# Kernel optimization log

Measured on AMD Instinct MI355X. Metric: run time of the kernel, lower is better.

## Reference

```python
import jax, jax.numpy as jnp
import numpy as np

P_PARTS = 6
NUM_CLASSES = 50000
BATCH = 128
PART_DIM = 256
LABEL_SMOOTH = 0.1
MARGIN = 0.3
TEMP = 3.0
KL_CLAMP = 5.0
LAMBDA_GRAPH = 0.1
LAMBDA_TRI = 1.0
LAMBDA_ADV = 0.1
START_EPOCH = 20


def setup_inputs() -> dict:
    key = jax.random.key(0)
    ks = jax.random.split(key, 8)
    id_logits = jax.random.normal(ks[0], (P_PARTS, BATCH, NUM_CLASSES), dtype=jnp.float32)
    id_features = jax.random.normal(ks[1], (P_PARTS, BATCH, PART_DIM), dtype=jnp.float32)
    gray_features = jax.random.normal(ks[2], (P_PARTS, BATCH, PART_DIM), dtype=jnp.float32)
    # soft labels are probability distributions (teacher softmax outputs)
    soft_labels = jax.nn.softmax(jax.random.normal(ks[3], (P_PARTS, BATCH, NUM_CLASSES), dtype=jnp.float32), axis=-1)
    entropy_weights = jax.random.uniform(ks[4], (P_PARTS, BATCH), dtype=jnp.float32)
    adv_logits = jax.random.normal(ks[5], (P_PARTS, BATCH, 2), dtype=jnp.float32)
    labels = jax.random.randint(ks[6], (BATCH,), 0, 16, dtype=jnp.int64 if jax.config.jax_enable_x64 else jnp.int32)
    modality_labels = jax.random.randint(ks[7], (BATCH,), 0, 2, dtype=jnp.int64 if jax.config.jax_enable_x64 else jnp.int32)
    return {
        'id_logits': id_logits,
        'id_features': id_features,
        'gray_features': gray_features,
        'soft_labels': soft_labels,
        'entropy_weights': entropy_weights,
        'adv_logits': adv_logits,
        'labels': labels,
        'modality_labels': modality_labels,
        'current_epoch': 25,
    }


def _ce(logits, labels, smoothing):
    # torch CrossEntropyLoss with label_smoothing, mean reduction. logits: [B,C]
    logp = jax.nn.log_softmax(logits, axis=-1)
    nll = -jnp.take_along_axis(logp, labels[:, None], axis=-1)[:, 0]
    smooth = -jnp.mean(logp, axis=-1)
    return jnp.mean((1.0 - smoothing) * nll + smoothing * smooth)


def _triplet(feat, target_feat, labels, same):
    # euclidean cdist [B,B]
    sq = (jnp.sum(feat * feat, axis=1)[:, None]
          + jnp.sum(target_feat * target_feat, axis=1)[None, :]
          - 2.0 * feat @ target_feat.T)
    dist = jnp.sqrt(jnp.clip(sq, 0.0) + 1e-12)
    eq = labels[:, None] == labels[None, :]
    is_neg = ~eq
    is_pos = eq & (~jnp.eye(feat.shape[0], dtype=bool)) if same else eq
    # vectorized hard mining (replaces per-row python loop)
    dist_ap = jnp.where(is_pos.any(axis=1),
                        jnp.max(jnp.where(is_pos, dist, -jnp.inf), axis=1), 0.0)
    dist_an = jnp.where(is_neg.any(axis=1),
                        jnp.min(jnp.where(is_neg, dist, jnp.inf), axis=1), 1e6)
    # MarginRankingLoss with y=1: mean(relu(dist_ap - dist_an + margin))
    return jnp.mean(jnp.maximum(dist_ap - dist_an + MARGIN, 0.0))


def reference(id_logits, id_features, gray_features, soft_labels, entropy_weights,
              adv_logits, labels, modality_labels, current_epoch):
    P = id_logits.shape[0]
    # --- multi-part ID loss ---
    L_id = jnp.mean(jax.vmap(lambda lg: _ce(lg, labels, LABEL_SMOOTH))(id_logits))
    # --- triplet on L2-normalized concatenated part features ---
    feat = jnp.concatenate(list(id_features), axis=1)  # [B, P*D]
    feat = feat / jnp.linalg.norm(feat, axis=1, keepdims=True)
    L_tri = _triplet(feat, feat, labels, same=True)
    feat_gray = jnp.concatenate(list(gray_features), axis=1)
    feat_gray = feat_gray / jnp.linalg.norm(feat_gray, axis=1, keepdims=True)
    L_trans = _triplet(feat, feat_gray, labels, same=False)
    L_tri = L_tri + 0.5 * L_trans
    # --- graph distillation (KL) ---
    if current_epoch >= START_EPOCH:
        logp = jax.nn.log_softmax(id_logits / TEMP, axis=-1)  # [P,B,C]
        kl = jnp.sum(soft_labels * (jnp.log(soft_labels) - logp), axis=-1)  # [P,B]
        kl = jnp.minimum(kl, KL_CLAMP)
        L_graph = jnp.sum(jnp.mean(kl * entropy_weights, axis=1)) * (TEMP ** 2) / P
    else:
        L_graph = jnp.float32(0.0)
    # --- adversarial CE ---
    logp_adv = jax.nn.log_softmax(adv_logits, axis=-1)  # [P,B,2]
    nll_adv = -jnp.take_along_axis(logp_adv, modality_labels[None, :, None], axis=-1)[..., 0]
    L_adv = jnp.mean(jnp.mean(nll_adv, axis=1))
    total = L_id + LAMBDA_TRI * L_tri + LAMBDA_GRAPH * L_graph + LAMBDA_ADV * L_adv
    return total
```

## Files before the change

kernel.cpp:

```cpp
#include <hip/hip_runtime.h>

#define NCLS   50000
#define NC4    12500
#define BATCH  128
#define PPARTS 6
#define NROWS  768
#define FD     1536
#define NCHUNK 5
#define C4     2500

__device__ __forceinline__ float wave_sum(float v) {
#pragma unroll
  for (int off = 32; off > 0; off >>= 1) v += __shfl_xor(v, off, 64);
  return v;
}

__global__ __launch_bounds__(128) void chunk_k(
    const float* __restrict__ X, const float* __restrict__ S,
    const int* __restrict__ labels, float* __restrict__ P) {
  const int gid = blockIdx.x;
  const int row = gid / NCHUNK;
  const int ch  = gid - row * NCHUNK;
  const int b   = row & (BATCH - 1);
  const int t   = threadIdx.x;
  const size_t base = (size_t)row * NCLS;
  const float4* x4 = (const float4*)(X + base) + ch * C4;
  const float4* s4 = (const float4*)(S + base) + ch * C4;
  const float i3 = 1.0f / 3.0f;

  float xl = 0.0f;
  if (ch == 0 && t == 0) xl = X[base + labels[b]];

  float m = -1e30f, e1 = 0.0f, e2 = 0.0f;
  float sx = 0.0f, ss = 0.0f, ssl = 0.0f, ssx = 0.0f;

  float4 xa = make_float4(0.f, 0.f, 0.f, 0.f), sa = xa, xb = xa, sb = xa;
  if (t < C4) { xa = x4[t]; sa = s4[t]; }
  if (t + 128 < C4) { xb = x4[t + 128]; sb = s4[t + 128]; }

  for (int i = t; i < C4; i += 128) {
    const int ip = i + 256;
    float4 xc = make_float4(0.f, 0.f, 0.f, 0.f), sc = xc;
    if (ip < C4) { xc = x4[ip]; sc = s4[ip]; }

    {
      const float x0 = xa.x, x1 = xa.y, x2 = xa.z, x3 = xa.w;
      const float s0 = sa.x, s1 = sa.y, s2 = sa.z, s3 = sa.w;
      const float mx = fmaxf(fmaxf(x0, x1), fmaxf(x2, x3));
      const float nm = fmaxf(m, mx);
      const float r3 = __expf((m - nm) * i3);
      const float r  = r3 * r3 * r3;
      const float u0 = __expf((x0 - nm) * i3);
      const float u1 = __expf((x1 - nm) * i3);
      const float u2 = __expf((x2 - nm) * i3);
      const float u3 = __expf((x3 - nm) * i3);
      e2 = e2 * r3 + ((u0 + u1) + (u2 + u3));
      float q0 = u0 * u0, q1 = u1 * u1, q2 = u2 * u2, q3 = u3 * u3;
      e1 = e1 * r + ((q0 * u0 + q1 * u1) + (q2 * u2 + q3 * u3));
      m = nm;
      sx += ((x0 + x1) + (x2 + x3));
      ss += ((s0 + s1) + (s2 + s3));
      ssl = fmaf(s0, __logf(s0), ssl);
      ssl = fmaf(s1, __logf(s1), ssl);
      ssl = fmaf(s2, __logf(s2), ssl);
      ssl = fmaf(s3, __logf(s3), ssl);
      ssx = fmaf(s0, x0, ssx);
      ssx = fmaf(s1, x1, ssx);
      ssx = fmaf(s2, x2, ssx);
      ssx = fmaf(s3, x3, ssx);
    }

    xa = xb; sa = sb;
    xb = xc; sb = sc;
  }

#pragma unroll
  for (int off = 32; off > 0; off >>= 1) {
    float mo  = __shfl_xor(m, off, 64);
    float e1o = __shfl_xor(e1, off, 64);
    float e2o = __shfl_xor(e2, off, 64);
    float nm = fmaxf(m, mo);
    e1 = e1 * __expf(m - nm) + e1o * __expf(mo - nm);
    e2 = e2 * __expf((m - nm) * i3) + e2o * __expf((mo - nm) * i3);
    m = nm;
    sx  += __shfl_xor(sx, off, 64);
    ss  += __shfl_xor(ss, off, 64);
    ssl += __shfl_xor(ssl, off, 64);
    ssx += __shfl_xor(ssx, off, 64);
  }

  __shared__ float rm[2], re1[2], re2[2], rsx[2], rss[2], rssl[2], rssx[2];
  const int lane = t & 63, wid = t >> 6;
  if (lane == 0) {
    rm[wid] = m; re1[wid] = e1; re2[wid] = e2;
    rsx[wid] = sx; rss[wid] = ss; rssl[wid] = ssl; rssx[wid] = ssx;
  }
  __syncthreads();
  if (t == 0) {
    float M = rm[0], E1 = re1[0], E2 = re2[0];
    float nm = fmaxf(M, rm[1]);
    E1 = E1 * __expf(M - nm) + re1[1] * __expf(rm[1] - nm);
    E2 = E2 * __expf((M - nm) * i3) + re2[1] * __expf((rm[1] - nm) * i3);
    M = nm;
    float4* o = (float4*)(P + (size_t)gid * 8);
    o[0] = make_float4(M, E1, E2, rsx[0] + rsx[1]);
    o[1] = make_float4(rss[0] + rss[1], rssl[0] + rssl[1],
                       rssx[0] + rssx[1], xl);
  }
}

__global__ __launch_bounds__(256) void normalize_k(
    const float* __restrict__ idf, const float* __restrict__ grayf,
    float* __restrict__ Fn, float* __restrict__ Gn) {
  const int src = blockIdx.x >> 7;
  const int b = blockIdx.x & (BATCH - 1);
  const int t = threadIdx.x;
  const float* in = src ? grayf : idf;
  float* out = src ? Gn : Fn;

  float v[6];
  float sq = 0.0f;
#pragma unroll
  for (int k = 0; k < 6; ++k) {
    v[k] = in[((k * BATCH + b) << 8) + t];
    sq = fmaf(v[k], v[k], sq);
  }
  sq = wave_sum(sq);
  __shared__ float wsum[4];
  __shared__ float inv_s;
  const int lane = t & 63, wid = t >> 6;
  if (lane == 0) wsum[wid] = sq;
  __syncthreads();
  if (t == 0) inv_s = 1.0f / sqrtf(wsum[0] + wsum[1] + wsum[2] + wsum[3]);
  __syncthreads();
  float inv = inv_s;
#pragma unroll
  for (int k = 0; k < 6; ++k)
    out[b * FD + (k << 8) + t] = v[k] * inv;
}

__global__ __launch_bounds__(256) void dist_k(
    const float* __restrict__ Fn, const float* __restrict__ Gn,
    float* __restrict__ D) {
  const int z = blockIdx.z;
  const float* Bm = z ? Gn : Fn;
  const int i0 = blockIdx.y * 16, j0 = blockIdx.x * 16;
  const int tx = threadIdx.x, ty = threadIdx.y;
  __shared__ float As[16][17], Bs[16][17];
  float acc = 0.0f;
  for (int k0 = 0; k0 < FD; k0 += 16) {
    As[ty][tx] = Fn[(i0 + ty) * FD + k0 + tx];
    Bs[ty][tx] = Bm[(j0 + ty) * FD + k0 + tx];
    __syncthreads();
#pragma unroll
    for (int k = 0; k < 16; ++k) acc = fmaf(As[ty][k], Bs[tx][k], acc);
    __syncthreads();
  }
  float sq = fmaxf(2.0f - 2.0f * acc, 0.0f) + 1e-12f;
  D[z * BATCH * BATCH + (i0 + ty) * BATCH + j0 + tx] = sqrtf(sq);
}

__global__ __launch_bounds__(256) void final_k(
    const float* __restrict__ P, const float* __restrict__ W,
    const float* __restrict__ D, const float* __restrict__ advl,
    const int* __restrict__ labels, const int* __restrict__ mod,
    const int* __restrict__ epoch, float* __restrict__ out) {
  const int t = threadIdx.x;
  const float i3 = 1.0f / 3.0f;
  __shared__ int slab[BATCH];
  if (t < BATCH) slab[t] = labels[t];

  float ce = 0.0f, klw = 0.0f;
#pragma unroll
  for (int k = 0; k < 3; ++k) {
    const int row = t + k * 256;
    const float* p = P + (size_t)row * NCHUNK * 8;
    float M = p[0], E1 = p[1], E2 = p[2], SX = p[3];
    float SS = p[4], SSL = p[5], SSX = p[6];
    const float xl = p[7];
#pragma unroll
    for (int ch = 1; ch < NCHUNK; ++ch) {
      const float* q = p + ch * 8;
      float mo = q[0];
      float nm = fmaxf(M, mo);
      E1 = E1 * __expf(M - nm) + q[1] * __expf(mo - nm);
      E2 = E2 * __expf((M - nm) * i3) + q[2] * __expf((mo - nm) * i3);
      M = nm;
      SX += q[3]; SS += q[4]; SSL += q[5]; SSX += q[6];
    }
    float logZ  = M + __logf(E1);
    float logZT = M * i3 + __logf(E2);
    ce += 0.9f * (logZ - xl) + 0.1f * (logZ - SX * (1.0f / NCLS));
    float kl = SSL - SSX * i3 + logZT * SS;
    klw += fminf(kl, 5.0f) * W[row];
  }

  float adv = 0.0f;
#pragma unroll
  for (int k = 0; k < 3; ++k) {
    const int r = t + k * 256;
    const int b = r & (BATCH - 1);
    float l0 = advl[2 * r], l1 = advl[2 * r + 1];
    float mx = fmaxf(l0, l1);
    float lse = mx + __logf(__expf(l0 - mx) + __expf(l1 - mx));
    adv += lse - (mod[b] ? l1 : l0);
  }

  __syncthreads();
  float l1s = 0.0f, l2s = 0.0f;
  if (t < BATCH) {
    const int lb = slab[t];
    const float* d1 = D + t * BATCH;
    const float* d2 = D + BATCH * BATCH + t * BATCH;
    float ap1 = -1e30f, an1 = 1e30f, ap2 = -1e30f, an2 = 1e30f;
    int hasp1 = 0, hasn = 0, hasp2 = 0;
    for (int j = 0; j < BATCH; ++j) {
      bool eq = (slab[j] == lb);
      float v1 = d1[j], v2 = d2[j];
      if (eq) {
        hasp2 = 1; ap2 = fmaxf(ap2, v2);
        if (j != t) { hasp1 = 1; ap1 = fmaxf(ap1, v1); }
      } else {
        hasn = 1; an1 = fminf(an1, v1); an2 = fminf(an2, v2);
      }
    }
    float dap1 = hasp1 ? ap1 : 0.0f;
    float dan1 = hasn ? an1 : 1e6f;
    l1s = fmaxf(dap1 - dan1 + 0.3f, 0.0f);
    float dap2 = hasp2 ? ap2 : 0.0f;
    float dan2 = hasn ? an2 : 1e6f;
    l2s = fmaxf(dap2 - dan2 + 0.3f, 0.0f);
  }

  ce  = wave_sum(ce);
  klw = wave_sum(klw);
  adv = wave_sum(adv);
  l1s = wave_sum(l1s);
  l2s = wave_sum(l2s);
  __shared__ float r0[4], r1[4], r2[4], r3[4], r4[4];
  const int lane = t & 63, wid = t >> 6;
  if (lane == 0) { r0[wid]=ce; r1[wid]=klw; r2[wid]=adv; r3[wid]=l1s; r4[wid]=l2s; }
  __syncthreads();
  if (t == 0) {
    float CE  = r0[0] + r0[1] + r0[2] + r0[3];
    float KLW = r1[0] + r1[1] + r1[2] + r1[3];
    float ADV = r2[0] + r2[1] + r2[2] + r2[3];
    float T1  = r3[0] + r3[1] + r3[2] + r3[3];
    float T2  = r4[0] + r4[1] + r4[2] + r4[3];
    float L_id    = CE * (1.0f / NROWS);
    float L_tri   = (T1 + 0.5f * T2) * (1.0f / BATCH);
    float L_graph = (epoch[0] >= 20) ? KLW * (9.0f / 768.0f) : 0.0f;
    float L_adv   = ADV * (1.0f / NROWS);
    out[0] = L_id + L_tri + 0.1f * L_graph + 0.1f * L_adv;
  }
}

extern "C" void kernel_launch(void* const* d_in, const int* in_sizes, int n_in,
                              void* d_out, int out_size, void* d_ws, size_t ws_size,
                              hipStream_t stream) {
  (void)in_sizes; (void)n_in; (void)out_size; (void)ws_size;
  const float* id_logits = (const float*)d_in[0];
  const float* id_feat   = (const float*)d_in[1];
  const float* gray_feat = (const float*)d_in[2];
  const float* soft      = (const float*)d_in[3];
  const float* entw      = (const float*)d_in[4];
  const float* advl      = (const float*)d_in[5];
  const int*   labels    = (const int*)d_in[6];
  const int*   modality  = (const int*)d_in[7];
  const int*   epoch     = (const int*)d_in[8];
  float* out = (float*)d_out;

  float* P  = (float*)d_ws;
  float* Fn = P + NROWS * NCHUNK * 8;
  float* Gn = Fn + BATCH * FD;
  float* D  = Gn + BATCH * FD;

  chunk_k<<<NROWS * NCHUNK, 128, 0, stream>>>(id_logits, soft, labels, P);
  normalize_k<<<256, 256, 0, stream>>>(id_feat, gray_feat, Fn, Gn);
  dist_k<<<dim3(8, 8, 2), dim3(16, 16), 0, stream>>>(Fn, Gn, D);
  final_k<<<1, 256, 0, stream>>>(P, entw, D, advl, labels, modality, epoch, out);
}
```

Baseline: 409.1 us.

## Stream logits through LDS with async global_load_lds pipeline per wave

The chunk reduction kernel now gives each wave its own contiguous slice of a row and fetches it with global_load_lds into a 4-deep LDS ring buffer, using explicit vmcnt waits to keep three tiles in flight. This replaces the register double-buffered float4 loads. The per-block cross-wave LDS reduction and __syncthreads are gone: each wave writes its own partial, so there are 10 partials per row and final_k merges them. The intent is deeper memory-level parallelism on a bandwidth-bound streaming pass, at the cost of hand-managed waitcnt ordering and cache-policy bits that may be fragile.

Result: faster. 397.9 us (-2.7%).

```diff
diff --git a/kernel.cpp b/kernel.cpp
--- a/kernel.cpp
+++ b/kernel.cpp
@@ -7,7 +7,18 @@
 #define NROWS  768
 #define FD     1536
 #define NCHUNK 5
-#define C4     2500
+#define NPART  10
+#define WF4    1250
+#define NTILE  19
+#define TAILF4 34
+#define DEPTH  4
+
+typedef float f32x4 __attribute__((ext_vector_type(4)));
+
+#define GL2LDS(gp, lp, aux)                                                    \
+  __builtin_amdgcn_global_load_lds(                                            \
+      (const __attribute__((address_space(1))) void*)(gp),                     \
+      (__attribute__((address_space(3))) void*)(lp), 16, 0, (aux))
 
 __device__ __forceinline__ float wave_sum(float v) {
 #pragma unroll
@@ -20,58 +31,87 @@
     const int* __restrict__ labels, float* __restrict__ P) {
   const int gid = blockIdx.x;
   const int row = gid / NCHUNK;
-  const int ch  = gid - row * NCHUNK;
+  const int sp  = gid - row * NCHUNK;
   const int b   = row & (BATCH - 1);
   const int t   = threadIdx.x;
+  const int lane = t & 63, wid = t >> 6;
   const size_t base = (size_t)row * NCLS;
-  const float4* x4 = (const float4*)(X + base) + ch * C4;
-  const float4* s4 = (const float4*)(S + base) + ch * C4;
+  const f32x4* xg4 = (const f32x4*)(X + base) + sp * (WF4 * 2) + wid * WF4;
+  const f32x4* sg4 = (const f32x4*)(S + base) + sp * (WF4 * 2) + wid * WF4;
   const float i3 = 1.0f / 3.0f;
 
+  __shared__ f32x4 XL[2][DEPTH][64];
+  __shared__ f32x4 SL[2][DEPTH][64];
+
   float xl = 0.0f;
-  if (ch == 0 && t == 0) xl = X[base + labels[b]];
+  if (sp == 0 && t == 0) xl = X[base + labels[b]];
 
   float m = -1e30f, e1 = 0.0f, e2 = 0.0f;
   float sx = 0.0f, ss = 0.0f, ssl = 0.0f, ssx = 0.0f;
 
-  float4 xa = make_float4(0.f, 0.f, 0.f, 0.f), sa = xa, xb = xa, sb = xa;
-  if (t < C4) { xa = x4[t]; sa = s4[t]; }
-  if (t + 128 < C4) { xb = x4[t + 128]; sb = s4[t + 128]; }
-
-  for (int i = t; i < C4; i += 128) {
-    const int ip = i + 256;
-    float4 xc = make_float4(0.f, 0.f, 0.f, 0.f), sc = xc;
-    if (ip < C4) { xc = x4[ip]; sc = s4[ip]; }
-
-    {
-      const float x0 = xa.x, x1 = xa.y, x2 = xa.z, x3 = xa.w;
-      const float s0 = sa.x, s1 = sa.y, s2 = sa.z, s3 = sa.w;
-      const float mx = fmaxf(fmaxf(x0, x1), fmaxf(x2, x3));
-      const float nm = fmaxf(m, mx);
-      const float r3 = __expf((m - nm) * i3);
-      const float r  = r3 * r3 * r3;
-      const float u0 = __expf((x0 - nm) * i3);
-      const float u1 = __expf((x1 - nm) * i3);
-      const float u2 = __expf((x2 - nm) * i3);
-      const float u3 = __expf((x3 - nm) * i3);
-      e2 = e2 * r3 + ((u0 + u1) + (u2 + u3));
-      float q0 = u0 * u0, q1 = u1 * u1, q2 = u2 * u2, q3 = u3 * u3;
-      e1 = e1 * r + ((q0 * u0 + q1 * u1) + (q2 * u2 + q3 * u3));
-      m = nm;
-      sx += ((x0 + x1) + (x2 + x3));
-      ss += ((s0 + s1) + (s2 + s3));
-      ssl = fmaf(s0, __logf(s0), ssl);
-      ssl = fmaf(s1, __logf(s1), ssl);
-      ssl = fmaf(s2, __logf(s2), ssl);
-      ssl = fmaf(s3, __logf(s3), ssl);
-      ssx = fmaf(s0, x0, ssx);
-      ssx = fmaf(s1, x1, ssx);
-      ssx = fmaf(s2, x2, ssx);
-      ssx = fmaf(s3, x3, ssx);
-    }
-
-    xa = xb; sa = sb;
-    xb = xc; sb = sc;
+  auto proc = [&](f32x4 xv, f32x4 sv) {
+    const float x0 = xv.x, x1 = xv.y, x2 = xv.z, x3 = xv.w;
+    const float s0 = sv.x, s1 = sv.y, s2 = sv.z, s3 = sv.w;
+    const float mx = fmaxf(fmaxf(x0, x1), fmaxf(x2, x3));
+    const float nm = fmaxf(m, mx);
+    const float r3 = __expf((m - nm) * i3);
+    const float r  = r3 * r3 * r3;
+    const float u0 = __expf((x0 - nm) * i3);
+    const float u1 = __expf((x1 - nm) * i3);
+    const float u2 = __expf((x2 - nm) * i3);
+    const float u3 = __expf((x3 - nm) * i3);
+    e2 = e2 * r3 + ((u0 + u1) + (u2 + u3));
+    float q0 = u0 * u0, q1 = u1 * u1, q2 = u2 * u2, q3 = u3 * u3;
+    e1 = e1 * r + ((q0 * u0 + q1 * u1) + (q2 * u2 + q3 * u3));
+    m = nm;
+    sx += ((x0 + x1) + (x2 + x3));
+    ss += ((s0 + s1) + (s2 + s3));
+    ssl = fmaf(s0, __logf(s0), ssl);
+    ssl = fmaf(s1, __logf(s1), ssl);
+    ssl = fmaf(s2, __logf(s2), ssl);
+    ssl = fmaf(s3, __logf(s3), ssl);
+    ssx = fmaf(s0, x0, ssx);
+    ssx = fmaf(s1, x1, ssx);
+    ssx = fmaf(s2, x2, ssx);
+    ssx = fmaf(s3, x3, ssx);
+  };
+
+  auto stage = [&](int tile) {
+    const int slot = tile & (DEPTH - 1);
+    GL2LDS(xg4 + tile * 64 + lane, &XL[wid][slot][0], 2);
+    GL2LDS(sg4 + tile * 64 + lane, &SL[wid][slot][0], 0);
+  };
+
+  auto tilecomp = [&](int slot) {
+    const f32x4 xv = XL[wid][slot][lane];
+    const f32x4 sv = SL[wid][slot][lane];
+    proc(xv, sv);
+  };
+
+  stage(0); stage(1); stage(2);
+
+#pragma unroll 4
+  for (int ti = 0; ti < NTILE - 3; ++ti) {
+    asm volatile("s_waitcnt lgkmcnt(0)" ::: "memory");
+    stage(ti + 3);
+    asm volatile("s_waitcnt vmcnt(6)" ::: "memory");
+    __builtin_amdgcn_sched_barrier(0);
+    tilecomp(ti & (DEPTH - 1));
+  }
+  asm volatile("s_waitcnt vmcnt(4)" ::: "memory");
+  __builtin_amdgcn_sched_barrier(0);
+  tilecomp((NTILE - 3) & (DEPTH - 1));
+  asm volatile("s_waitcnt vmcnt(2)" ::: "memory");
+  __builtin_amdgcn_sched_barrier(0);
+  tilecomp((NTILE - 2) & (DEPTH - 1));
+  asm volatile("s_waitcnt vmcnt(0)" ::: "memory");
+  __builtin_amdgcn_sched_barrier(0);
+  tilecomp((NTILE - 1) & (DEPTH - 1));
+
+  if (lane < TAILF4) {
+    f32x4 xv = __builtin_nontemporal_load(xg4 + NTILE * 64 + lane);
+    f32x4 sv = sg4[NTILE * 64 + lane];
+    proc(xv, sv);
   }
 
 #pragma unroll
@@ -89,23 +129,10 @@
     ssx += __shfl_xor(ssx, off, 64);
   }
 
-  __shared__ float rm[2], re1[2], re2[2], rsx[2], rss[2], rssl[2], rssx[2];
-  const int lane = t & 63, wid = t >> 6;
   if (lane == 0) {
-    rm[wid] = m; re1[wid] = e1; re2[wid] = e2;
-    rsx[wid] = sx; rss[wid] = ss; rssl[wid] = ssl; rssx[wid] = ssx;
-  }
-  __syncthreads();
-  if (t == 0) {
-    float M = rm[0], E1 = re1[0], E2 = re2[0];
-    float nm = fmaxf(M, rm[1]);
-    E1 = E1 * __expf(M - nm) + re1[1] * __expf(rm[1] - nm);
-    E2 = E2 * __expf((M - nm) * i3) + re2[1] * __expf((rm[1] - nm) * i3);
-    M = nm;
-    float4* o = (float4*)(P + (size_t)gid * 8);
-    o[0] = make_float4(M, E1, E2, rsx[0] + rsx[1]);
-    o[1] = make_float4(rss[0] + rss[1], rssl[0] + rssl[1],
-                       rssx[0] + rssx[1], xl);
+    float4* o = (float4*)(P + (size_t)(row * NPART + sp * 2 + wid) * 8);
+    o[0] = make_float4(m, e1, e2, sx);
+    o[1] = make_float4(ss, ssl, ssx, xl);
   }
 }
 
@@ -174,12 +201,12 @@
 #pragma unroll
   for (int k = 0; k < 3; ++k) {
     const int row = t + k * 256;
-    const float* p = P + (size_t)row * NCHUNK * 8;
+    const float* p = P + (size_t)row * NPART * 8;
     float M = p[0], E1 = p[1], E2 = p[2], SX = p[3];
     float SS = p[4], SSL = p[5], SSX = p[6];
     const float xl = p[7];
 #pragma unroll
-    for (int ch = 1; ch < NCHUNK; ++ch) {
+    for (int ch = 1; ch < NPART; ++ch) {
       const float* q = p + ch * 8;
       float mo = q[0];
       float nm = fmaxf(M, mo);
@@ -271,7 +298,7 @@
   float* out = (float*)d_out;
 
   float* P  = (float*)d_ws;
-  float* Fn = P + NROWS * NCHUNK * 8;
+  float* Fn = P + NROWS * NPART * 8;
   float* Gn = Fn + BATCH * FD;
   float* D  = Gn + BATCH * FD;
 
```
